# Performance work log

Hardware: AMD Instinct MI355X
Metric: run time of the kernel (lower is better)

Reference implementation:

```python
import jax, jax.numpy as jnp
import numpy as np

B, T, D = 4, 2048, 1024
H, KD, VD = 16, 64, 64  # num_heads, key_dim, value_dim; H*KD == D


def setup_inputs() -> dict:
    key = jax.random.key(0)
    ks = jax.random.split(key, 10)
    s = 0.02
    return {
        "q_in": jax.random.normal(ks[0], (B, T, D), jnp.float32),
        "v_in": jax.random.normal(ks[1], (B, T, D), jnp.float32),
        "Wq": jax.random.normal(ks[2], (D, H * KD), jnp.float32) * s,
        "bq": jnp.zeros((H * KD,), jnp.float32),
        "Wk": jax.random.normal(ks[3], (D, H * KD), jnp.float32) * s,
        "bk": jnp.zeros((H * KD,), jnp.float32),
        "Wv": jax.random.normal(ks[4], (D, H * VD), jnp.float32) * s,
        "bv": jnp.zeros((H * VD,), jnp.float32),
        "Wo": jax.random.normal(ks[5], (H * VD, D), jnp.float32) * s,
        "bo": jnp.zeros((D,), jnp.float32),
    }


def reference(q_in, v_in, Wq, bq, Wk, bk, Wv, bv, Wo, bo):
    # QKV projections (key defaults to value input)
    q = q_in @ Wq + bq                      # [B,T,H*KD]
    k = v_in @ Wk + bk                      # [B,T,H*KD]
    v = v_in @ Wv + bv                      # [B,T,H*VD]
    q = q.reshape(B, T, H, KD)
    k = k.reshape(B, T, H, KD)
    v = v.reshape(B, T, H, VD)
    # scaled dot-product attention, scores materialized as [B,H,Tq,Tv]
    q = q / jnp.sqrt(jnp.asarray(KD, q.dtype))
    scores = jnp.einsum('bqnh,bvnh->bnqv', q, k)
    weights = jax.nn.softmax(scores, axis=-1)
    out = jnp.einsum('bnqv,bvnh->bqnh', weights, v)  # [B,Tq,H,VD]
    out = out.reshape(B, T, H * VD)
    return out @ Wo + bo                    # [B,T,D]
```

## Files before the change

### kernel.cpp

```cpp
#include <hip/hip_runtime.h>

#define BATCH  4
#define T_SEQ  2048
#define NH     16
#define DMODEL 1024
#define HD     64

typedef float    f32x4 __attribute__((ext_vector_type(4)));
typedef _Float16 f16x8 __attribute__((ext_vector_type(8)));
typedef _Float16 f16x4 __attribute__((ext_vector_type(4)));
typedef __fp16   h16x2 __attribute__((ext_vector_type(2)));

#define LOG2E 1.44269504088896f

__device__ __forceinline__ void lds_load16(const void* g, void* l) {
  __builtin_amdgcn_global_load_lds((const __attribute__((address_space(1))) void*)g,
                                   (__attribute__((address_space(3))) void*)l, 16, 0, 0);
}

__device__ __forceinline__ f16x4 pack4_f16(float a, float b, float c, float d) {
  union { h16x2 h[2]; f16x4 f; } u;
  u.h[0] = __builtin_amdgcn_cvt_pkrtz(a, b);
  u.h[1] = __builtin_amdgcn_cvt_pkrtz(c, d);
  return u.f;
}

#define MEMFENCE asm volatile("" ::: "memory")
#define WAITVM4  asm volatile("s_waitcnt vmcnt(4)" ::: "memory")
#define WAITVM0  asm volatile("s_waitcnt vmcnt(0)" ::: "memory")
#define PH_ENTER do { MEMFENCE; __builtin_amdgcn_s_barrier(); \
                      asm volatile("s_waitcnt lgkmcnt(0)" ::: "memory"); } while (0)
#define PH_EXIT  do { MEMFENCE; __builtin_amdgcn_s_barrier(); MEMFENCE; } while (0)

__global__ __launch_bounds__(256) void cast2_f32_to_f16(
    const float* __restrict__ a, const float* __restrict__ bsrc,
    _Float16* __restrict__ oa, _Float16* __restrict__ ob, int n4) {
  const float* in = blockIdx.y ? bsrc : a;
  _Float16* out = blockIdx.y ? ob : oa;
  int i = blockIdx.x * 256 + threadIdx.x;
  if (i < n4) {
    float4 v = ((const float4*)in)[i];
    f16x4 o = { (_Float16)v.x, (_Float16)v.y, (_Float16)v.z, (_Float16)v.w };
    ((f16x4*)out)[i] = o;
  }
}

__global__ __launch_bounds__(256) void transcast_w4(
    const float* __restrict__ W0, const float* __restrict__ W1,
    const float* __restrict__ W2, const float* __restrict__ W3,
    _Float16* __restrict__ T0, _Float16* __restrict__ T1,
    _Float16* __restrict__ T2, _Float16* __restrict__ T3) {
  const float* W; _Float16* Wt;
  switch (blockIdx.z) {
    case 0: W = W0; Wt = T0; break;
    case 1: W = W1; Wt = T1; break;
    case 2: W = W2; Wt = T2; break;
    default: W = W3; Wt = T3; break;
  }
  __shared__ float L[64][65];
  const int n0 = blockIdx.x * 64, k0 = blockIdx.y * 64;
  const int tx = threadIdx.x & 15, ty = threadIdx.x >> 4;
#pragma unroll
  for (int i = 0; i < 4; ++i) {
    float4 v = *(const float4*)&W[(size_t)(k0 + ty + 16 * i) * DMODEL + n0 + tx * 4];
    L[ty + 16 * i][tx * 4 + 0] = v.x;
    L[ty + 16 * i][tx * 4 + 1] = v.y;
    L[ty + 16 * i][tx * 4 + 2] = v.z;
    L[ty + 16 * i][tx * 4 + 3] = v.w;
  }
  __syncthreads();
#pragma unroll
  for (int i = 0; i < 4; ++i) {
    int n = n0 + ty + 16 * i;
    f16x4 o;
#pragma unroll
    for (int j = 0; j < 4; ++j) o[j] = (_Float16)L[tx * 4 + j][ty + 16 * i];
    *(f16x4*)&Wt[(size_t)n * DMODEL + k0 + tx * 4] = o;
  }
}

__device__ __forceinline__ void gemm256_body(
    const _Float16* __restrict__ A, const _Float16* __restrict__ Wt,
    const float* __restrict__ bias, void* __restrict__ Cout, float scale,
    int mode, _Float16* As0, _Float16* Bs0, _Float16* As1, _Float16* Bs1) {
  const int K = DMODEL;
  const int lane = threadIdx.x & 63, wave = threadIdx.x >> 6;
  const int m16 = lane & 15, quad = lane >> 4;
  const int wm = wave & 1;
  const int wn = wave >> 1;

  const int lin = blockIdx.x + blockIdx.y * gridDim.x;
  const int wg = (lin & 7) * 16 + (lin >> 3);
  const int m0 = (wg >> 2) * 256;
  const int n0 = (wg & 3) * 256;

  const int kof = (wave & 1) * 32 + quad * 8;
  const _Float16* aB[2][2]; const _Float16* bB[2][2];
#pragma unroll
  for (int h = 0; h < 2; ++h)
#pragma unroll
    for (int j = 0; j < 2; ++j) {
      int r = h * 128 + (wave >> 1) * 16 + 64 * j + m16;
      aB[h][j] = A  + (size_t)(m0 + r) * K + kof;
      bB[h][j] = Wt + (size_t)(n0 + r) * K + kof;
    }

  auto stageA = [&](_Float16* Ab, int h, int t) {
#pragma unroll
    for (int j = 0; j < 2; ++j)
      lds_load16(aB[h][j] + t * 64, Ab + (h * 16 + wave + 8 * j) * 512 + lane * 8);
  };
  auto stageB = [&](_Float16* Bb, int h, int t) {
#pragma unroll
    for (int j = 0; j < 2; ++j)
      lds_load16(bB[h][j] + t * 64, Bb + (h * 16 + wave + 8 * j) * 512 + lane * 8);
  };
  auto rdA = [&](const _Float16* Ab, int mi, int kh) {
    return *(const f16x8*)(Ab + (((wm * 8 + mi) * 2 + kh) * 64 + lane) * 8);
  };
  auto rdB = [&](const _Float16* Bb, int ni, int kh) {
    return *(const f16x8*)(Bb + (((wn * 4 + ni) * 2 + kh) * 64 + lane) * 8);
  };

  f32x4 acc[8][4] = {};

  auto tile_step = [&](int t, _Float16* Ac, const _Float16* Bc, _Float16* Bn) {
    f16x8 a03[4][2], a47[4][2], b01[2][2], b23[2][2];
#pragma unroll
    for (int mi = 0; mi < 4; ++mi) { a03[mi][0] = rdA(Ac, mi, 0); a03[mi][1] = rdA(Ac, mi, 1); }
#pragma unroll
    for (int ni = 0; ni < 2; ++ni) { b01[ni][0] = rdB(Bc, ni, 0); b01[ni][1] = rdB(Bc, ni, 1); }
    if (t < 15) stageB(Bn, 0, t + 1);
    PH_ENTER;
    __builtin_amdgcn_s_setprio(1);
#pragma unroll
    for (int mi = 0; mi < 4; ++mi)
#pragma unroll
      for (int ni = 0; ni < 2; ++ni)
#pragma unroll
        for (int kh = 0; kh < 2; ++kh)
          acc[mi][ni] = __builtin_amdgcn_mfma_f32_16x16x32_f16(a03[mi][kh], b01[ni][kh], acc[mi][ni], 0, 0, 0);
    __builtin_amdgcn_s_setprio(0);
    PH_EXIT;
#pragma unroll
    for (int ni = 0; ni < 2; ++ni) { b23[ni][0] = rdB(Bc, 2 + ni, 0); b23[ni][1] = rdB(Bc, 2 + ni, 1); }
    if (t < 15) stageB(Bn, 1, t + 1);
    PH_ENTER;
    __builtin_amdgcn_s_setprio(1);
#pragma unroll
    for (int mi = 0; mi < 4; ++mi)
#pragma unroll
      for (int ni = 0; ni < 2; ++ni)
#pragma unroll
        for (int kh = 0; kh < 2; ++kh)
          acc[mi][2 + ni] = __builtin_amdgcn_mfma_f32_16x16x32_f16(a03[mi][kh], b23[ni][kh], acc[mi][2 + ni], 0, 0, 0);
    __builtin_amdgcn_s_setprio(0);
    PH_EXIT;
#pragma unroll
    for (int mi = 0; mi < 4; ++mi) { a47[mi][0] = rdA(Ac, 4 + mi, 0); a47[mi][1] = rdA(Ac, 4 + mi, 1); }
    PH_ENTER;
    __builtin_amdgcn_s_setprio(1);
#pragma unroll
    for (int mi = 0; mi < 4; ++mi)
#pragma unroll
      for (int ni = 0; ni < 2; ++ni)
#pragma unroll
        for (int kh = 0; kh < 2; ++kh)
          acc[4 + mi][ni] = __builtin_amdgcn_mfma_f32_16x16x32_f16(a47[mi][kh], b01[ni][kh], acc[4 + mi][ni], 0, 0, 0);
    __builtin_amdgcn_s_setprio(0);
    PH_EXIT;
    if (t < 14) { stageA(Ac, 0, t + 2); stageA(Ac, 1, t + 2); }
    PH_ENTER;
    __builtin_amdgcn_s_setprio(1);
#pragma unroll
    for (int mi = 0; mi < 4; ++mi)
#pragma unroll
      for (int ni = 0; ni < 2; ++ni)
#pragma unroll
        for (int kh = 0; kh < 2; ++kh)
          acc[4 + mi][2 + ni] = __builtin_amdgcn_mfma_f32_16x16x32_f16(a47[mi][kh], b23[ni][kh], acc[4 + mi][2 + ni], 0, 0, 0);
    __builtin_amdgcn_s_setprio(0);
    if (t < 14)       WAITVM4;
    else if (t == 14) WAITVM0;
    MEMFENCE; __builtin_amdgcn_s_barrier(); MEMFENCE;
  };

  stageA(As0, 0, 0); stageA(As0, 1, 0);
  stageB(Bs0, 0, 0); stageB(Bs0, 1, 0);
  stageA(As1, 0, 1); stageA(As1, 1, 1);
  WAITVM4;
  MEMFENCE; __builtin_amdgcn_s_barrier(); MEMFENCE;

  for (int tp = 0; tp < 8; ++tp) {
    tile_step(2 * tp,     As0, Bs0, Bs1);
    tile_step(2 * tp + 1, As1, Bs1, Bs0);
  }

  float bv[4];
#pragma unroll
  for (int ni = 0; ni < 4; ++ni) bv[ni] = bias[n0 + wn * 64 + ni * 16 + m16];

  if (mode == 2) {
#pragma unroll
    for (int mi = 0; mi < 8; ++mi)
#pragma unroll
      for (int ni = 0; ni < 4; ++ni) {
        int row = m0 + wm * 128 + mi * 16 + quad * 4;
        int col = n0 + wn * 64 + ni * 16 + m16;
        int bb = row >> 11, tt = row & (T_SEQ - 1);
        int hh = col >> 6, dd = col & 63;
        f16x4 pv = pack4_f16(acc[mi][ni][0] + bv[ni], acc[mi][ni][1] + bv[ni],
                             acc[mi][ni][2] + bv[ni], acc[mi][ni][3] + bv[ni]);
        *(f16x4*)&((_Float16*)Cout)[(((size_t)bb * NH + hh) * HD + dd) * T_SEQ + tt] = pv;
      }
  } else if (mode == 0) {
#pragma unroll
    for (int mi = 0; mi < 8; ++mi)
#pragma unroll
      for (int r = 0; r < 4; ++r) {
        int row = m0 + wm * 128 + mi * 16 + quad * 4 + r;
#pragma unroll
        for (int ni = 0; ni < 4; ++ni) {
          int col = n0 + wn * 64 + ni * 16 + m16;
          float v = (acc[mi][ni][r] + bv[ni]) * scale;
          ((_Float16*)Cout)[(size_t)row * DMODEL + col] = (_Float16)v;
        }
      }
  } else {
#pragma unroll
    for (int mi = 0; mi < 8; ++mi)
#pragma unroll
      for (int r = 0; r < 4; ++r) {
        int row = m0 + wm * 128 + mi * 16 + quad * 4 + r;
#pragma unroll
        for (int ni = 0; ni < 4; ++ni) {
          int col = n0 + wn * 64 + ni * 16 + m16;
          ((float*)Cout)[(size_t)row * DMODEL + col] = acc[mi][ni][r] + bv[ni];
        }
      }
  }
}

__global__ __launch_bounds__(512, 2) void gemm_qkv(
    const _Float16* __restrict__ Aq, const _Float16* __restrict__ Av,
    const _Float16* __restrict__ Wq, const _Float16* __restrict__ Wk,
    const _Float16* __restrict__ Wv,
    const float* __restrict__ bq, const float* __restrict__ bk,
    const float* __restrict__ bv,
    _Float16* __restrict__ Cq, _Float16* __restrict__ Ck, _Float16* __restrict__ Cv) {
  __shared__ _Float16 As[2][16384], Bs[2][16384];
  const _Float16* A; const _Float16* Wt; const float* bias; _Float16* C;
  float scale; int mode;
  if (blockIdx.z == 0)      { A = Aq; Wt = Wq; bias = bq; C = Cq; scale = 0.125f * LOG2E; mode = 0; }
  else if (blockIdx.z == 1) { A = Av; Wt = Wk; bias = bk; C = Ck; scale = 1.f; mode = 0; }
  else                      { A = Av; Wt = Wv; bias = bv; C = Cv; scale = 1.f; mode = 2; }
  gemm256_body(A, Wt, bias, C, scale, mode, As[0], Bs[0], As[1], Bs[1]);
}

__global__ __launch_bounds__(512, 2) void gemm_out(
    const _Float16* __restrict__ A, const _Float16* __restrict__ Wt,
    const float* __restrict__ bias, float* __restrict__ Cout) {
  __shared__ _Float16 As[2][16384], Bs[2][16384];
  gemm256_body(A, Wt, bias, Cout, 1.f, 3, As[0], Bs[0], As[1], Bs[1]);
}

__global__ __launch_bounds__(256, 2) void attn_mfma(
    const _Float16* __restrict__ Q, const _Float16* __restrict__ Kb,
    const _Float16* __restrict__ Vt, _Float16* __restrict__ O) {
  __shared__ _Float16 Ks[64 * 64], Vs[64 * 64];
  __shared__ _Float16 Ps[4 * 4096];

  const int lane = threadIdx.x & 63, wave = threadIdx.x >> 6;
  const int m16 = lane & 15, quad = lane >> 4;
  const int h = blockIdx.x;
  const int q0 = blockIdx.y * 256;
  const int b = blockIdx.z;
  const int wq = wave * 64;
  const int wbase = wave * 4096;

  f16x8 qf[4][2];
#pragma unroll
  for (int mi = 0; mi < 4; ++mi)
#pragma unroll
    for (int ki = 0; ki < 2; ++ki) {
      int q = q0 + wq + mi * 16 + m16;
      qf[mi][ki] = *(const f16x8*)(Q + (((size_t)b * T_SEQ + q) * NH + h) * HD + ki * 32 + quad * 8);
    }

  const _Float16 *kp[2], *vp[2];
#pragma unroll
  for (int i = 0; i < 2; ++i) {
    int g = wave * 128 + i * 64 + lane;
    int tk = (g >> 7) * 16 + (g & 15);
    int dkof = ((g >> 6) & 1) * 32 + ((g >> 4) & 3) * 8;
    kp[i] = Kb + (((size_t)b * T_SEQ + tk) * NH + h) * HD + dkof;
    int dvof = (g >> 7) * 16 + (g & 15);
    int tv = ((g >> 6) & 1) * 32 + ((g >> 4) & 3) * 8;
    vp[i] = Vt + (((size_t)b * NH + h) * HD + dvof) * T_SEQ + tv;
  }

  int pw[4][4];
#pragma unroll
  for (int mi = 0; mi < 4; ++mi)
#pragma unroll
    for (int nt = 0; nt < 4; ++nt) {
      int kt = nt >> 1;
      int q8 = ((nt & 1) << 1) | (quad >> 1);
      pw[mi][nt] = wbase + ((mi * 2 + kt) * 64 + q8 * 16 + m16) * 8 + (quad & 1) * 4;
    }

  const f16x8 onef = {(_Float16)1, (_Float16)1, (_Float16)1, (_Float16)1,
                      (_Float16)1, (_Float16)1, (_Float16)1, (_Float16)1};

  f32x4 o_acc[4][4] = {};
  f32x4 l_acc[4] = {};

  for (int kv = 0; kv < T_SEQ; kv += 64) {
    __syncthreads();
#pragma unroll
    for (int i = 0; i < 2; ++i) {
      lds_load16(kp[i] + (size_t)kv * (NH * HD), Ks + (wave * 2 + i) * 512);
      lds_load16(vp[i] + kv, Vs + (wave * 2 + i) * 512);
    }
    __syncthreads();

    f32x4 st[4][4] = {};
#pragma unroll
    for (int nt = 0; nt < 4; ++nt)
#pragma unroll
      for (int ki = 0; ki < 2; ++ki) {
        f16x8 kf = *(const f16x8*)(Ks + ((nt * 2 + ki) * 64 + lane) * 8);
#pragma unroll
        for (int mi = 0; mi < 4; ++mi)
          st[mi][nt] = __builtin_amdgcn_mfma_f32_16x16x32_f16(kf, qf[mi][ki], st[mi][nt], 0, 0, 0);
      }

#pragma unroll
    for (int mi = 0; mi < 4; ++mi)
#pragma unroll
      for (int nt = 0; nt < 4; ++nt) {
        f16x4 p = pack4_f16(__builtin_amdgcn_exp2f(st[mi][nt][0]),
                            __builtin_amdgcn_exp2f(st[mi][nt][1]),
                            __builtin_amdgcn_exp2f(st[mi][nt][2]),
                            __builtin_amdgcn_exp2f(st[mi][nt][3]));
        *(f16x4*)(Ps + pw[mi][nt]) = p;
      }

#pragma unroll
    for (int kt = 0; kt < 2; ++kt) {
      f16x8 pf[4];
#pragma unroll
      for (int mi = 0; mi < 4; ++mi) {
        pf[mi] = *(const f16x8*)(Ps + wbase + ((mi * 2 + kt) * 64 + lane) * 8);
        l_acc[mi] = __builtin_amdgcn_mfma_f32_16x16x32_f16(pf[mi], onef, l_acc[mi], 0, 0, 0);
      }
#pragma unroll
      for (int nd = 0; nd < 4; ++nd) {
        f16x8 vf = *(const f16x8*)(Vs + ((nd * 2 + kt) * 64 + lane) * 8);
#pragma unroll
        for (int mi = 0; mi < 4; ++mi)
          o_acc[mi][nd] = __builtin_amdgcn_mfma_f32_16x16x32_f16(pf[mi], vf, o_acc[mi][nd], 0, 0, 0);
      }
    }
  }

#pragma unroll
  for (int mi = 0; mi < 4; ++mi)
#pragma unroll
    for (int r = 0; r < 4; ++r) {
      float inv = 1.f / l_acc[mi][r];
      int q = q0 + wq + mi * 16 + quad * 4 + r;
#pragma unroll
      for (int nd = 0; nd < 4; ++nd) {
        int d = nd * 16 + m16;
        O[(((size_t)b * T_SEQ + q) * NH + h) * HD + d] = (_Float16)(o_acc[mi][nd][r] * inv);
      }
    }
}

extern "C" void kernel_launch(void* const* d_in, const int* in_sizes, int n_in,
                              void* d_out, int out_size, void* d_ws, size_t ws_size,
                              hipStream_t stream) {
  const float* q_in = (const float*)d_in[0];
  const float* v_in = (const float*)d_in[1];
  const float* Wq   = (const float*)d_in[2];
  const float* bq   = (const float*)d_in[3];
  const float* Wk   = (const float*)d_in[4];
  const float* bk   = (const float*)d_in[5];
  const float* Wv   = (const float*)d_in[6];
  const float* bv   = (const float*)d_in[7];
  const float* Wo   = (const float*)d_in[8];
  const float* bo   = (const float*)d_in[9];
  float* out = (float*)d_out;

  const size_t MB = 1u << 20;
  char* ws = (char*)d_ws;
  _Float16* q16  = (_Float16*)(ws);
  _Float16* v16  = (_Float16*)(ws + 16 * MB);
  _Float16* qbuf = (_Float16*)(ws + 32 * MB);
  _Float16* kbuf = (_Float16*)(ws + 48 * MB);
  _Float16* vtb  = (_Float16*)(ws + 64 * MB);
  _Float16* Wqt  = (_Float16*)(ws + 80 * MB);
  _Float16* Wkt  = (_Float16*)(ws + 82 * MB);
  _Float16* Wvt  = (_Float16*)(ws + 84 * MB);
  _Float16* Wot  = (_Float16*)(ws + 86 * MB);

  const int n4 = BATCH * T_SEQ * DMODEL / 4;
  cast2_f32_to_f16<<<dim3(n4 / 256, 2), 256, 0, stream>>>(q_in, v_in, q16, v16, n4);

  transcast_w4<<<dim3(16, 16, 4), 256, 0, stream>>>(Wq, Wk, Wv, Wo, Wqt, Wkt, Wvt, Wot);

  gemm_qkv<<<dim3(4, 32, 3), 512, 0, stream>>>(q16, v16, Wqt, Wkt, Wvt, bq, bk, bv,
                                               qbuf, kbuf, vtb);

  attn_mfma<<<dim3(16, 8, 4), 256, 0, stream>>>(qbuf, kbuf, vtb, qbuf);

  gemm_out<<<dim3(4, 32), 512, 0, stream>>>(qbuf, Wot, bo, out);
}
```

Baseline: 337.8 us.

## Double-buffer attention K/V loads, add MFMA priority, retile output GEMM to 128x128

The attention kernel now double-buffers K/V tiles in LDS. It prefetches the next tile while computing the current one, with a single barrier per iteration, and raises wave priority around the MFMA bursts. The output projection drops the shared 256x256 GEMM body for a simpler 128x128-tile, 256-thread kernel on a 512-block grid, aiming for more blocks and better occupancy. The LDS destination in the staging lambdas loses its per-lane offset, which fits the global_load_lds semantics where the LDS base is wave-uniform. The non-pipelined single-buffer out GEMM may lose some latency hiding.

```diff
diff --git a/kernel.cpp b/kernel.cpp
--- a/kernel.cpp
+++ b/kernel.cpp
@@ -108,12 +108,12 @@
   auto stageA = [&](_Float16* Ab, int h, int t) {
 #pragma unroll
     for (int j = 0; j < 2; ++j)
-      lds_load16(aB[h][j] + t * 64, Ab + (h * 16 + wave + 8 * j) * 512 + lane * 8);
+      lds_load16(aB[h][j] + t * 64, Ab + (h * 16 + wave + 8 * j) * 512);
   };
   auto stageB = [&](_Float16* Bb, int h, int t) {
 #pragma unroll
     for (int j = 0; j < 2; ++j)
-      lds_load16(bB[h][j] + t * 64, Bb + (h * 16 + wave + 8 * j) * 512 + lane * 8);
+      lds_load16(bB[h][j] + t * 64, Bb + (h * 16 + wave + 8 * j) * 512);
   };
   auto rdA = [&](const _Float16* Ab, int mi, int kh) {
     return *(const f16x8*)(Ab + (((wm * 8 + mi) * 2 + kh) * 64 + lane) * 8);
@@ -257,17 +257,69 @@
   gemm256_body(A, Wt, bias, C, scale, mode, As[0], Bs[0], As[1], Bs[1]);
 }
 
-__global__ __launch_bounds__(512, 2) void gemm_out(
+__global__ __launch_bounds__(256, 3) void gemm_out(
     const _Float16* __restrict__ A, const _Float16* __restrict__ Wt,
     const float* __restrict__ bias, float* __restrict__ Cout) {
-  __shared__ _Float16 As[2][16384], Bs[2][16384];
-  gemm256_body(A, Wt, bias, Cout, 1.f, 3, As[0], Bs[0], As[1], Bs[1]);
+  __shared__ _Float16 As[128 * 64], Bs[128 * 64];
+  const int K = DMODEL;
+  const int lane = threadIdx.x & 63, wave = threadIdx.x >> 6;
+  const int bid = blockIdx.x + blockIdx.y * gridDim.x;
+  const int m0 = ((bid & 7) * 8 + ((bid >> 3) & 7)) * 128;
+  const int n0 = (bid >> 6) * 128;
+  const int wr = (wave & 1) * 4, wc = (wave >> 1) * 4;
+  const int m16 = lane & 15, quad = lane >> 4;
+
+  const _Float16* ap[4]; const _Float16* bp[4];
+#pragma unroll
+  for (int j = 0; j < 4; ++j) {
+    int g = wave * 4 + j;
+    ap[j] = A  + (size_t)(m0 + (g >> 1) * 16 + m16) * K + (g & 1) * 32 + quad * 8;
+    bp[j] = Wt + (size_t)(n0 + (g >> 1) * 16 + m16) * K + (g & 1) * 32 + quad * 8;
+  }
+
+  f32x4 acc[4][4] = {};
+
+  for (int k0 = 0; k0 < 1024; k0 += 64) {
+    __syncthreads();
+#pragma unroll
+    for (int j = 0; j < 4; ++j) {
+      lds_load16(ap[j] + k0, As + (wave * 4 + j) * 512);
+      lds_load16(bp[j] + k0, Bs + (wave * 4 + j) * 512);
+    }
+    __syncthreads();
+#pragma unroll
+    for (int s = 0; s < 2; ++s) {
+      f16x8 bf[4];
+#pragma unroll
+      for (int ni = 0; ni < 4; ++ni)
+        bf[ni] = *(const f16x8*)(Bs + (((wc + ni) * 2 + s) * 64 + lane) * 8);
+#pragma unroll
+      for (int mi = 0; mi < 4; ++mi) {
+        f16x8 af = *(const f16x8*)(As + (((wr + mi) * 2 + s) * 64 + lane) * 8);
+#pragma unroll
+        for (int ni = 0; ni < 4; ++ni)
+          acc[mi][ni] = __builtin_amdgcn_mfma_f32_16x16x32_f16(af, bf[ni], acc[mi][ni], 0, 0, 0);
+      }
+    }
+  }
+
+#pragma unroll
+  for (int mi = 0; mi < 4; ++mi)
+#pragma unroll
+    for (int r = 0; r < 4; ++r) {
+      int row = m0 + (wr + mi) * 16 + quad * 4 + r;
+#pragma unroll
+      for (int ni = 0; ni < 4; ++ni) {
+        int col = n0 + (wc + ni) * 16 + m16;
+        Cout[(size_t)row * DMODEL + col] = acc[mi][ni][r] + bias[col];
+      }
+    }
 }
 
 __global__ __launch_bounds__(256, 2) void attn_mfma(
     const _Float16* __restrict__ Q, const _Float16* __restrict__ Kb,
     const _Float16* __restrict__ Vt, _Float16* __restrict__ O) {
-  __shared__ _Float16 Ks[64 * 64], Vs[64 * 64];
+  __shared__ _Float16 Ks[2][64 * 64], Vs[2][64 * 64];
   __shared__ _Float16 Ps[4 * 4096];
 
   const int lane = threadIdx.x & 63, wave = threadIdx.x >> 6;
@@ -299,6 +351,14 @@
     vp[i] = Vt + (((size_t)b * NH + h) * HD + dvof) * T_SEQ + tv;
   }
 
+  auto stageKV = [&](int c, int kv) {
+#pragma unroll
+    for (int i = 0; i < 2; ++i) {
+      lds_load16(kp[i] + (size_t)kv * (NH * HD), Ks[c] + (wave * 2 + i) * 512);
+      lds_load16(vp[i] + kv, Vs[c] + (wave * 2 + i) * 512);
+    }
+  };
+
   int pw[4][4];
 #pragma unroll
   for (int mi = 0; mi < 4; ++mi)
@@ -315,24 +375,25 @@
   f32x4 o_acc[4][4] = {};
   f32x4 l_acc[4] = {};
 
-  for (int kv = 0; kv < T_SEQ; kv += 64) {
-    __syncthreads();
-#pragma unroll
-    for (int i = 0; i < 2; ++i) {
-      lds_load16(kp[i] + (size_t)kv * (NH * HD), Ks + (wave * 2 + i) * 512);
-      lds_load16(vp[i] + kv, Vs + (wave * 2 + i) * 512);
-    }
-    __syncthreads();
+  stageKV(0, 0);
+  WAITVM0;
+  MEMFENCE; __builtin_amdgcn_s_barrier(); MEMFENCE;
+
+  for (int t = 0; t < 32; ++t) {
+    const int c = t & 1;
+    if (t < 31) stageKV(c ^ 1, (t + 1) * 64);
 
     f32x4 st[4][4] = {};
 #pragma unroll
     for (int nt = 0; nt < 4; ++nt)
 #pragma unroll
       for (int ki = 0; ki < 2; ++ki) {
-        f16x8 kf = *(const f16x8*)(Ks + ((nt * 2 + ki) * 64 + lane) * 8);
+        f16x8 kf = *(const f16x8*)(Ks[c] + ((nt * 2 + ki) * 64 + lane) * 8);
+        __builtin_amdgcn_s_setprio(1);
 #pragma unroll
         for (int mi = 0; mi < 4; ++mi)
           st[mi][nt] = __builtin_amdgcn_mfma_f32_16x16x32_f16(kf, qf[mi][ki], st[mi][nt], 0, 0, 0);
+        __builtin_amdgcn_s_setprio(0);
       }
 
 #pragma unroll
@@ -356,12 +417,17 @@
       }
 #pragma unroll
       for (int nd = 0; nd < 4; ++nd) {
-        f16x8 vf = *(const f16x8*)(Vs + ((nd * 2 + kt) * 64 + lane) * 8);
+        f16x8 vf = *(const f16x8*)(Vs[c] + ((nd * 2 + kt) * 64 + lane) * 8);
+        __builtin_amdgcn_s_setprio(1);
 #pragma unroll
         for (int mi = 0; mi < 4; ++mi)
           o_acc[mi][nd] = __builtin_amdgcn_mfma_f32_16x16x32_f16(pf[mi], vf, o_acc[mi][nd], 0, 0, 0);
-      }
-    }
+        __builtin_amdgcn_s_setprio(0);
+      }
+    }
+
+    WAITVM0;
+    MEMFENCE; __builtin_amdgcn_s_barrier(); MEMFENCE;
   }
 
 #pragma unroll
@@ -415,5 +481,5 @@
 
   attn_mfma<<<dim3(16, 8, 4), 256, 0, stream>>>(qbuf, kbuf, vtb, qbuf);
 
-  gemm_out<<<dim3(4, 32), 512, 0, stream>>>(qbuf, Wot, bo, out);
-}
+  gemm_out<<<dim3(8, 64), 256, 0, stream>>>(qbuf, Wot, bo, out);
+}
```

Measured after the change: 331.6 us. No clear change (-1.8%).
